# Kernel optimization log

Measured on AMD Instinct MI355X. Metric: run time of the kernel, lower is better.

## Reference

```python
import jax, jax.numpy as jnp
import numpy as np

BSZ, L, D = 8, 2048, 1024

def setup_inputs() -> dict:
    key = jax.random.key(0)
    k1, k2, k3, k4 = jax.random.split(key, 4)
    s = 1.0 / np.sqrt(D)
    return {
        "x":   jax.random.normal(k1, (BSZ, L, D), dtype=jnp.float32),
        "A":   jax.random.normal(k2, (D,), dtype=jnp.float32),
        "W_B": jax.random.normal(k3, (D, D), dtype=jnp.float32) * s,
        "b_B": jnp.zeros((D,), dtype=jnp.float32),
        "W_C": jax.random.normal(k4, (D, D), dtype=jnp.float32) * s,
        "b_C": jnp.zeros((D,), dtype=jnp.float32),
    }

def reference(x, A, W_B, b_B, W_C, b_C):
    # Precompute B(x_t) for all t in one GEMM: [B, L, D]
    Bx = jnp.einsum("bld,ed->ble", x, W_B) + b_B
    h0 = jnp.zeros((x.shape[0], x.shape[2]), dtype=x.dtype)

    def step(h, bx_t):
        h = jnp.tanh(A * h + bx_t)   # elementwise recurrence
        return h, h

    # scan over time: Bx -> [L, B, D]
    _, hs = jax.lax.scan(step, h0, jnp.swapaxes(Bx, 0, 1))
    # y_t = C(h_t), batched over all t: hs [L, B, D]
    y = jnp.einsum("lbd,ed->lbe", hs, W_C) + b_C
    return jnp.swapaxes(y, 0, 1)  # [B, L, D]
```

## Files before the change

kernel.cpp:

```cpp
#include <hip/hip_runtime.h>
#include <hip/hip_bf16.h>
#include <stdint.h>


using half8 = __attribute__((ext_vector_type(8))) _Float16;
using f32x4 = __attribute__((ext_vector_type(4))) float;

#define DEV __device__ __forceinline__

#if __has_builtin(__builtin_amdgcn_exp2f)
DEV float pexp(float x) { return __builtin_amdgcn_exp2f(x); }
constexpr float BX_SCALE = 2.8853900817779268f;
#else
DEV float pexp(float x) { return __expf(x); }
constexpr float BX_SCALE = 2.0f;
#endif

DEV ushort f2h(float x) {
  union { _Float16 f; ushort u; } c;
  c.f = (_Float16)x;
  return c.u;
}
DEV float h2f(ushort u) {
  union { ushort u; _Float16 f; } c;
  c.u = u;
  return (float)c.f;
}

DEV void gload_lds16(const void* g, void* l) {
  __builtin_amdgcn_global_load_lds((const __attribute__((address_space(1))) void*)g,
                                   (__attribute__((address_space(3))) void*)l,
                                   16, 0, 0);
}

__global__ void k_convert_all(const float* __restrict__ X, const float* __restrict__ WB,
                              const float* __restrict__ WC,
                              ushort* __restrict__ xh, ushort* __restrict__ xl,
                              ushort* __restrict__ wbh, ushort* __restrict__ wbl,
                              ushort* __restrict__ wch, int n4x, int n4w) {
  const int stride = gridDim.x * blockDim.x;
  const int total = n4x + 2 * n4w;
  for (int i = blockIdx.x * blockDim.x + threadIdx.x; i < total; i += stride) {
    if (i < n4x) {
      float4 v = reinterpret_cast<const float4*>(X)[i];
      ushort4 hv, lv;
      hv.x = f2h(v.x); lv.x = f2h(v.x - h2f(hv.x));
      hv.y = f2h(v.y); lv.y = f2h(v.y - h2f(hv.y));
      hv.z = f2h(v.z); lv.z = f2h(v.z - h2f(hv.z));
      hv.w = f2h(v.w); lv.w = f2h(v.w - h2f(hv.w));
      reinterpret_cast<ushort4*>(xh)[i] = hv;
      reinterpret_cast<ushort4*>(xl)[i] = lv;
    } else if (i < n4x + n4w) {
      const int j = i - n4x;
      float4 v = reinterpret_cast<const float4*>(WB)[j];
      ushort4 hv, lv;
      hv.x = f2h(v.x); lv.x = f2h(v.x - h2f(hv.x));
      hv.y = f2h(v.y); lv.y = f2h(v.y - h2f(hv.y));
      hv.z = f2h(v.z); lv.z = f2h(v.z - h2f(hv.z));
      hv.w = f2h(v.w); lv.w = f2h(v.w - h2f(hv.w));
      reinterpret_cast<ushort4*>(wbh)[j] = hv;
      reinterpret_cast<ushort4*>(wbl)[j] = lv;
    } else {
      const int j = i - n4x - n4w;
      float4 v = reinterpret_cast<const float4*>(WC)[j];
      ushort4 hv;
      hv.x = f2h(v.x); hv.y = f2h(v.y);
      hv.z = f2h(v.z); hv.w = f2h(v.w);
      reinterpret_cast<ushort4*>(wch)[j] = hv;
    }
  }
}

template <int SPLIT, int SCALE, int MINWAVES>
__global__ __launch_bounds__(256, MINWAVES)
void k_gemm_bt(const ushort* __restrict__ Ah, const ushort* __restrict__ Al,
               const ushort* __restrict__ Bh, const ushort* __restrict__ Bl,
               const float* __restrict__ bias, const float* __restrict__ Avec,
               float* __restrict__ C, int M, int N, int K) {
  constexpr int NMAT = SPLIT ? 4 : 2;
  __shared__ __align__(1024) ushort lds[NMAT * 128 * 64];
  ushort* sAh = lds;
  ushort* sAl = lds + (SPLIT ? 8192 : 0);
  ushort* sBh = lds + (SPLIT ? 16384 : 8192);
  ushort* sBl = lds + (SPLIT ? 24576 : 8192);

  const int t = threadIdx.x;
  const int lane = t & 63;
  const int w = t >> 6;
  const int wm = w >> 1, wn = w & 1;

  int bm, bn;
  {
    const int l = blockIdx.y * 8 + blockIdx.x;
    const int xcd = l & 7, s = l >> 3;
    bm = ((s >> 3) << 3) | xcd;
    bn = s & 7;
  }

  const int lr = lane & 15;
  const int lk = (lane >> 4) << 3;

  const ushort* gA_h = Ah + (size_t)(bm * 128) * K;
  const ushort* gA_l = SPLIT ? (Al + (size_t)(bm * 128) * K) : gA_h;
  const ushort* gB_h = Bh + (size_t)(bn * 128) * K;
  const ushort* gB_l = SPLIT ? (Bl + (size_t)(bn * 128) * K) : gB_h;

  f32x4 acc[4][4];
#pragma unroll
  for (int i = 0; i < 4; ++i)
#pragma unroll
    for (int j = 0; j < 4; ++j)
#pragma unroll
      for (int r = 0; r < 4; ++r) acc[i][j][r] = 0.f;

  auto stage = [&](int kt) {
    const int k0 = kt * 64;
#pragma unroll
    for (int i = 0; i < 4; ++i) {
      const int lin16 = i * 256 + t;
      const int lb = lin16 << 4;
      const int row = lb >> 7;
      const int srcb = (lb & 127) ^ ((row & 7) << 4);
      const size_t goff = (size_t)row * K + (size_t)(k0 + (srcb >> 1));
      const int lidx = i * 2048 + w * 512;
      gload_lds16(gA_h + goff, sAh + lidx);
      if (SPLIT) gload_lds16(gA_l + goff, sAl + lidx);
      gload_lds16(gB_h + goff, sBh + lidx);
      if (SPLIT) gload_lds16(gB_l + goff, sBl + lidx);
    }
  };

  auto ldfrag = [&](const ushort* s, int row, int kc) -> half8 {
    const int byte = (row << 7) + (((kc << 1) ^ ((row & 7) << 4)));
    return *reinterpret_cast<const half8*>(reinterpret_cast<const char*>(s) + byte);
  };

  const int NT = K / 64;
  stage(0);
  for (int kt = 0; kt < NT; ++kt) {
    __syncthreads();
#pragma unroll
    for (int kk = 0; kk < 2; ++kk) {
      half8 ah[4], bh[4], al[4], bl[4];
      const int kc = kk * 32 + lk;
#pragma unroll
      for (int i = 0; i < 4; ++i) {
        const int row = wm * 64 + i * 16 + lr;
        ah[i] = ldfrag(sAh, row, kc);
        if (SPLIT) al[i] = ldfrag(sAl, row, kc);
      }
#pragma unroll
      for (int j = 0; j < 4; ++j) {
        const int row = wn * 64 + j * 16 + lr;
        bh[j] = ldfrag(sBh, row, kc);
        if (SPLIT) bl[j] = ldfrag(sBl, row, kc);
      }
#pragma unroll
      for (int i = 0; i < 4; ++i)
#pragma unroll
        for (int j = 0; j < 4; ++j) {
          acc[i][j] = __builtin_amdgcn_mfma_f32_16x16x32_f16(ah[i], bh[j], acc[i][j], 0, 0, 0);
          if (SPLIT) {
            acc[i][j] = __builtin_amdgcn_mfma_f32_16x16x32_f16(al[i], bh[j], acc[i][j], 0, 0, 0);
            acc[i][j] = __builtin_amdgcn_mfma_f32_16x16x32_f16(ah[i], bl[j], acc[i][j], 0, 0, 0);
          }
        }
    }
    __syncthreads();
    if (kt + 1 < NT) stage(kt + 1);
  }

  float* Cb = C + (size_t)(bm * 128) * N + bn * 128;
#pragma unroll
  for (int i = 0; i < 4; ++i)
#pragma unroll
    for (int j = 0; j < 4; ++j) {
      const int col = wn * 64 + j * 16 + lr;
      float bv = bias[bn * 128 + col];
      if (SCALE) bv += Avec[bn * 128 + col];
#pragma unroll
      for (int r = 0; r < 4; ++r) {
        const int rowt = wm * 64 + i * 16 + ((lane >> 4) << 2) + r;
        float o = acc[i][j][r] + bv;
        if (SCALE) o *= BX_SCALE;
        Cb[(size_t)rowt * N + col] = o;
      }
    }
}

__global__ __launch_bounds__(64)
void k_recurrence(const float* __restrict__ Bx2, const float* __restrict__ Avec,
                  ushort* __restrict__ Hout) {
  const int tid = blockIdx.x * 64 + threadIdx.x;
  const int b = tid >> 10;
  const int d = tid & 1023;
  const float na2 = -2.f * BX_SCALE * Avec[d];
  const float* bx = Bx2 + (size_t)b * 2048 * 1024 + d;
  ushort* ho = Hout + (size_t)b * 2048 * 1024 + d;

  constexpr int P = 32;
  constexpr int NC = 2048 / P;
  float cA[P], cB[P];
#pragma unroll
  for (int i = 0; i < P; ++i) cA[i] = bx[(size_t)i * 1024];
#pragma unroll
  for (int i = 0; i < P; ++i) cB[i] = bx[(size_t)(P + i) * 1024];

  float r = 0.5f;
  for (int c = 0; c < NC; c += 2) {
#pragma unroll
    for (int i = 0; i < P; ++i) {
      const float u2 = fmaf(na2, r, cA[i]);
      r = __builtin_amdgcn_rcpf(pexp(u2) + 1.f);
      ho[(size_t)(c * P + i) * 1024] = f2h(fmaf(-2.f, r, 1.f));
    }
    if (c + 2 < NC) {
#pragma unroll
      for (int i = 0; i < P; ++i) cA[i] = bx[(size_t)((c + 2) * P + i) * 1024];
    }
#pragma unroll
    for (int i = 0; i < P; ++i) {
      const float u2 = fmaf(na2, r, cB[i]);
      r = __builtin_amdgcn_rcpf(pexp(u2) + 1.f);
      ho[(size_t)((c + 1) * P + i) * 1024] = f2h(fmaf(-2.f, r, 1.f));
    }
    if (c + 3 < NC) {
#pragma unroll
      for (int i = 0; i < P; ++i) cB[i] = bx[(size_t)((c + 3) * P + i) * 1024];
    }
  }
}

extern "C" void kernel_launch(void* const* d_in, const int* in_sizes, int n_in,
                              void* d_out, int out_size, void* d_ws, size_t ws_size,
                              hipStream_t stream) {
  const float* x   = (const float*)d_in[0];
  const float* A   = (const float*)d_in[1];
  const float* W_B = (const float*)d_in[2];
  const float* b_B = (const float*)d_in[3];
  const float* W_C = (const float*)d_in[4];
  const float* b_C = (const float*)d_in[5];
  float* y = (float*)d_out;

  const int Bsz = 8, L = 2048, D = 1024;
  const int M = Bsz * L;

  char* ws = (char*)d_ws;
  ushort* x_hi = (ushort*)(ws);
  ushort* x_lo = (ushort*)(ws + 33554432);
  ushort* wbh  = (ushort*)(ws + 67108864);
  ushort* wbl  = (ushort*)(ws + 69206016);
  ushort* wch  = (ushort*)(ws + 71303168);
  float*  Bx   = (float*)(ws + 73400320);
  ushort* h    = x_hi;

  k_convert_all<<<2048, 256, 0, stream>>>(x, W_B, W_C, x_hi, x_lo, wbh, wbl, wch,
                                          M * D / 4, D * D / 4);

  k_gemm_bt<1, 1, 2><<<dim3(8, M / 128), 256, 0, stream>>>(
      x_hi, x_lo, wbh, wbl, b_B, A, Bx, M, D, D);

  k_recurrence<<<(Bsz * D) / 64, 64, 0, stream>>>(Bx, A, h);

  k_gemm_bt<0, 0, 4><<<dim3(8, M / 128), 256, 0, stream>>>(
      h, (const ushort*)nullptr, wch, (const ushort*)nullptr, b_C,
      (const float*)nullptr, y, M, D, D);
}
```

Baseline: 230.1 us.

## Double-buffer LDS tiles with K=32 stages to overlap global loads with MFMA

Replaces the single-buffer K=64 staging loop with a two-buffer K=32 pipeline. The next tile is loaded straight into LDS while MFMAs run on the current one, and each iteration needs one barrier instead of two. The LDS layout is also reorganized: two rows are packed per 128-byte line with a new XOR swizzle, so the fragment reads match the narrower K tile. This should hide global load latency behind compute and cut barrier stalls. The cost is more loop iterations, each doing less MFMA work.

```diff
diff --git a/kernel.cpp b/kernel.cpp
--- a/kernel.cpp
+++ b/kernel.cpp
@@ -78,11 +78,7 @@
                const float* __restrict__ bias, const float* __restrict__ Avec,
                float* __restrict__ C, int M, int N, int K) {
   constexpr int NMAT = SPLIT ? 4 : 2;
-  __shared__ __align__(1024) ushort lds[NMAT * 128 * 64];
-  ushort* sAh = lds;
-  ushort* sAl = lds + (SPLIT ? 8192 : 0);
-  ushort* sBh = lds + (SPLIT ? 16384 : 8192);
-  ushort* sBl = lds + (SPLIT ? 24576 : 8192);
+  __shared__ __align__(1024) ushort lds[2 * NMAT * 4096];
 
   const int t = threadIdx.x;
   const int lane = t & 63;
@@ -98,7 +94,7 @@
   }
 
   const int lr = lane & 15;
-  const int lk = (lane >> 4) << 3;
+  const int kcb = (lane >> 4) << 4;
 
   const ushort* gA_h = Ah + (size_t)(bm * 128) * K;
   const ushort* gA_l = SPLIT ? (Al + (size_t)(bm * 128) * K) : gA_h;
@@ -113,61 +109,71 @@
 #pragma unroll
       for (int r = 0; r < 4; ++r) acc[i][j][r] = 0.f;
 
-  auto stage = [&](int kt) {
-    const int k0 = kt * 64;
+  auto stage = [&](int kt, int buf) {
+    const int k0 = kt * 32;
+    ushort* base = lds + buf * (NMAT * 4096);
+#pragma unroll
+    for (int i = 0; i < 2; ++i) {
+      const int lin16 = i * 256 + t;
+      const int line = lin16 >> 3;
+      const int row = (line << 1) | ((lin16 >> 2) & 1);
+      const int kb = ((lin16 & 3) << 4) ^ ((line & 3) << 4);
+      const size_t goff = (size_t)row * K + (size_t)(k0 + (kb >> 1));
+      const int dst = lin16 << 3;
+      gload_lds16(gA_h + goff, base + dst);
+      gload_lds16(gB_h + goff, base + (SPLIT ? 2 : 1) * 4096 + dst);
+      if (SPLIT) {
+        gload_lds16(gA_l + goff, base + 4096 + dst);
+        gload_lds16(gB_l + goff, base + 3 * 4096 + dst);
+      }
+    }
+  };
+
+  auto ldfrag = [&](const ushort* mat, int row) -> half8 {
+    const int line = row >> 1;
+    const int off = (line << 7) + ((row & 1) << 6) + (kcb ^ ((line & 3) << 4));
+    return *reinterpret_cast<const half8*>(reinterpret_cast<const char*>(mat) + off);
+  };
+
+  auto compute = [&](int buf) {
+    const ushort* base = lds + buf * (NMAT * 4096);
+    const ushort* sAh = base;
+    const ushort* sAl = base + 4096;
+    const ushort* sBh = base + (SPLIT ? 2 : 1) * 4096;
+    const ushort* sBl = base + 3 * 4096;
+
+    half8 ah[4], al[4], bh[4], bl[4];
 #pragma unroll
     for (int i = 0; i < 4; ++i) {
-      const int lin16 = i * 256 + t;
-      const int lb = lin16 << 4;
-      const int row = lb >> 7;
-      const int srcb = (lb & 127) ^ ((row & 7) << 4);
-      const size_t goff = (size_t)row * K + (size_t)(k0 + (srcb >> 1));
-      const int lidx = i * 2048 + w * 512;
-      gload_lds16(gA_h + goff, sAh + lidx);
-      if (SPLIT) gload_lds16(gA_l + goff, sAl + lidx);
-      gload_lds16(gB_h + goff, sBh + lidx);
-      if (SPLIT) gload_lds16(gB_l + goff, sBl + lidx);
-    }
+      const int r = wm * 64 + i * 16 + lr;
+      ah[i] = ldfrag(sAh, r);
+      if (SPLIT) al[i] = ldfrag(sAl, r);
+    }
+#pragma unroll
+    for (int j = 0; j < 4; ++j) {
+      const int r = wn * 64 + j * 16 + lr;
+      bh[j] = ldfrag(sBh, r);
+      if (SPLIT) bl[j] = ldfrag(sBl, r);
+    }
+#pragma unroll
+    for (int i = 0; i < 4; ++i)
+#pragma unroll
+      for (int j = 0; j < 4; ++j) {
+        acc[i][j] = __builtin_amdgcn_mfma_f32_16x16x32_f16(ah[i], bh[j], acc[i][j], 0, 0, 0);
+        if (SPLIT) {
+          acc[i][j] = __builtin_amdgcn_mfma_f32_16x16x32_f16(al[i], bh[j], acc[i][j], 0, 0, 0);
+          acc[i][j] = __builtin_amdgcn_mfma_f32_16x16x32_f16(ah[i], bl[j], acc[i][j], 0, 0, 0);
+        }
+      }
   };
 
-  auto ldfrag = [&](const ushort* s, int row, int kc) -> half8 {
-    const int byte = (row << 7) + (((kc << 1) ^ ((row & 7) << 4)));
-    return *reinterpret_cast<const half8*>(reinterpret_cast<const char*>(s) + byte);
-  };
-
-  const int NT = K / 64;
-  stage(0);
+  const int NT = K / 32;
+  stage(0, 0);
+  __syncthreads();
   for (int kt = 0; kt < NT; ++kt) {
+    if (kt + 1 < NT) stage(kt + 1, (kt + 1) & 1);
+    compute(kt & 1);
     __syncthreads();
-#pragma unroll
-    for (int kk = 0; kk < 2; ++kk) {
-      half8 ah[4], bh[4], al[4], bl[4];
-      const int kc = kk * 32 + lk;
-#pragma unroll
-      for (int i = 0; i < 4; ++i) {
-        const int row = wm * 64 + i * 16 + lr;
-        ah[i] = ldfrag(sAh, row, kc);
-        if (SPLIT) al[i] = ldfrag(sAl, row, kc);
-      }
-#pragma unroll
-      for (int j = 0; j < 4; ++j) {
-        const int row = wn * 64 + j * 16 + lr;
-        bh[j] = ldfrag(sBh, row, kc);
-        if (SPLIT) bl[j] = ldfrag(sBl, row, kc);
-      }
-#pragma unroll
-      for (int i = 0; i < 4; ++i)
-#pragma unroll
-        for (int j = 0; j < 4; ++j) {
-          acc[i][j] = __builtin_amdgcn_mfma_f32_16x16x32_f16(ah[i], bh[j], acc[i][j], 0, 0, 0);
-          if (SPLIT) {
-            acc[i][j] = __builtin_amdgcn_mfma_f32_16x16x32_f16(al[i], bh[j], acc[i][j], 0, 0, 0);
-            acc[i][j] = __builtin_amdgcn_mfma_f32_16x16x32_f16(ah[i], bl[j], acc[i][j], 0, 0, 0);
-          }
-        }
-    }
-    __syncthreads();
-    if (kt + 1 < NT) stage(kt + 1);
   }
 
   float* Cb = C + (size_t)(bm * 128) * N + bn * 128;
```

After: 248.5 us. 8.0% more time.

## Double-buffer LDS tiles in GEMM kernels with vmcnt-based prefetch pipelining

Applied to the files above, without the earlier changes.

Gives both GEMM kernels two LDS buffers and prefetches the tile two steps ahead. A partial s_waitcnt on vmcnt lets the next tile's global-to-LDS loads overlap MFMA compute on the current one, where the old loop had a full sync between load and use. This doubles LDS use per block (128KB for the split GEMM, 64KB for the plain one), so the launch-bounds occupancy hints are halved. The tradeoff is fewer resident waves in exchange for overlapping loads with compute.

```diff
diff --git a/kernel.cpp b/kernel.cpp
--- a/kernel.cpp
+++ b/kernel.cpp
@@ -78,11 +78,7 @@
                const float* __restrict__ bias, const float* __restrict__ Avec,
                float* __restrict__ C, int M, int N, int K) {
   constexpr int NMAT = SPLIT ? 4 : 2;
-  __shared__ __align__(1024) ushort lds[NMAT * 128 * 64];
-  ushort* sAh = lds;
-  ushort* sAl = lds + (SPLIT ? 8192 : 0);
-  ushort* sBh = lds + (SPLIT ? 16384 : 8192);
-  ushort* sBl = lds + (SPLIT ? 24576 : 8192);
+  __shared__ __align__(1024) ushort lds[2 * NMAT * 8192];
 
   const int t = threadIdx.x;
   const int lane = t & 63;
@@ -113,8 +109,9 @@
 #pragma unroll
       for (int r = 0; r < 4; ++r) acc[i][j][r] = 0.f;
 
-  auto stage = [&](int kt) {
+  auto stage = [&](int kt, int buf) {
     const int k0 = kt * 64;
+    ushort* base = lds + buf * (NMAT * 8192);
 #pragma unroll
     for (int i = 0; i < 4; ++i) {
       const int lin16 = i * 256 + t;
@@ -123,10 +120,10 @@
       const int srcb = (lb & 127) ^ ((row & 7) << 4);
       const size_t goff = (size_t)row * K + (size_t)(k0 + (srcb >> 1));
       const int lidx = i * 2048 + w * 512;
-      gload_lds16(gA_h + goff, sAh + lidx);
-      if (SPLIT) gload_lds16(gA_l + goff, sAl + lidx);
-      gload_lds16(gB_h + goff, sBh + lidx);
-      if (SPLIT) gload_lds16(gB_l + goff, sBl + lidx);
+      gload_lds16(gA_h + goff, base + lidx);
+      if (SPLIT) gload_lds16(gA_l + goff, base + 8192 + lidx);
+      gload_lds16(gB_h + goff, base + (SPLIT ? 2 : 1) * 8192 + lidx);
+      if (SPLIT) gload_lds16(gB_l + goff, base + 3 * 8192 + lidx);
     }
   };
 
@@ -135,10 +132,12 @@
     return *reinterpret_cast<const half8*>(reinterpret_cast<const char*>(s) + byte);
   };
 
-  const int NT = K / 64;
-  stage(0);
-  for (int kt = 0; kt < NT; ++kt) {
-    __syncthreads();
+  auto compute = [&](int buf) {
+    const ushort* base = lds + buf * (NMAT * 8192);
+    const ushort* sAh = base;
+    const ushort* sAl = base + 8192;
+    const ushort* sBh = base + (SPLIT ? 2 : 1) * 8192;
+    const ushort* sBl = base + 3 * 8192;
 #pragma unroll
     for (int kk = 0; kk < 2; ++kk) {
       half8 ah[4], bh[4], al[4], bl[4];
@@ -166,8 +165,24 @@
           }
         }
     }
-    __syncthreads();
-    if (kt + 1 < NT) stage(kt + 1);
+  };
+
+  const int NT = K / 64;
+  stage(0, 0);
+  stage(1, 1);
+  for (int kt = 0; kt < NT; ++kt) {
+    if (kt + 1 < NT) {
+      if (SPLIT) asm volatile("s_waitcnt vmcnt(16)" ::: "memory");
+      else       asm volatile("s_waitcnt vmcnt(8)" ::: "memory");
+    } else {
+      asm volatile("s_waitcnt vmcnt(0)" ::: "memory");
+    }
+    __builtin_amdgcn_s_barrier();
+    __builtin_amdgcn_sched_barrier(0);
+    compute(kt & 1);
+    __builtin_amdgcn_s_barrier();
+    __builtin_amdgcn_sched_barrier(0);
+    if (kt + 2 < NT) stage(kt + 2, kt & 1);
   }
 
   float* Cb = C + (size_t)(bm * 128) * N + bn * 128;
@@ -257,12 +272,12 @@
   k_convert_all<<<2048, 256, 0, stream>>>(x, W_B, W_C, x_hi, x_lo, wbh, wbl, wch,
                                           M * D / 4, D * D / 4);
 
-  k_gemm_bt<1, 1, 2><<<dim3(8, M / 128), 256, 0, stream>>>(
+  k_gemm_bt<1, 1, 1><<<dim3(8, M / 128), 256, 0, stream>>>(
       x_hi, x_lo, wbh, wbl, b_B, A, Bx, M, D, D);
 
   k_recurrence<<<(Bsz * D) / 64, 64, 0, stream>>>(Bx, A, h);
 
-  k_gemm_bt<0, 0, 4><<<dim3(8, M / 128), 256, 0, stream>>>(
+  k_gemm_bt<0, 0, 2><<<dim3(8, M / 128), 256, 0, stream>>>(
       h, (const ushort*)nullptr, wch, (const ushort*)nullptr, b_C,
       (const float*)nullptr, y, M, D, D);
 }
```

New measurement: 257.6 us. 11.9% more time.

## Pipeline time chunks so recurrence overlaps with both GEMMs in fused launches

Applied to the files above, without the earlier changes.

The sequence dimension is split into four 512-step chunks. One combined kernel runs three roles per launch: the recurrence on chunk c, the input GEMM on chunk c+1 and the output GEMM on chunk c-1. The recurrence carries its hidden state between launches through a workspace buffer. This hides the latency-bound serial scan behind the GEMM work. In exchange there are more launches, the recurrence blocks now share CUs with GEMM blocks, and launch bounds and register limits are shared across all roles.

```diff
diff --git a/kernel.cpp b/kernel.cpp
--- a/kernel.cpp
+++ b/kernel.cpp
@@ -71,14 +71,12 @@
   }
 }
 
-template <int SPLIT, int SCALE, int MINWAVES>
-__global__ __launch_bounds__(256, MINWAVES)
-void k_gemm_bt(const ushort* __restrict__ Ah, const ushort* __restrict__ Al,
-               const ushort* __restrict__ Bh, const ushort* __restrict__ Bl,
-               const float* __restrict__ bias, const float* __restrict__ Avec,
-               float* __restrict__ C, int M, int N, int K) {
-  constexpr int NMAT = SPLIT ? 4 : 2;
-  __shared__ __align__(1024) ushort lds[NMAT * 128 * 64];
+template <int SPLIT, int SCALE>
+DEV void gemm_role(const ushort* __restrict__ Ah, const ushort* __restrict__ Al,
+                   const ushort* __restrict__ Bh, const ushort* __restrict__ Bl,
+                   const float* __restrict__ bias, const float* __restrict__ Avec,
+                   float* __restrict__ C, int chunk, int g, ushort* lds) {
+  constexpr int K = 1024, N = 1024;
   ushort* sAh = lds;
   ushort* sAl = lds + (SPLIT ? 8192 : 0);
   ushort* sBh = lds + (SPLIT ? 16384 : 8192);
@@ -89,13 +87,10 @@
   const int w = t >> 6;
   const int wm = w >> 1, wn = w & 1;
 
-  int bm, bn;
-  {
-    const int l = blockIdx.y * 8 + blockIdx.x;
-    const int xcd = l & 7, s = l >> 3;
-    bm = ((s >> 3) << 3) | xcd;
-    bn = s & 7;
-  }
+  const int xcd = g & 7, s = g >> 3;
+  const int tc = (s & ~7) | xcd;
+  const int bn = s & 7;
+  const int bm = ((tc >> 2) << 4) + chunk * 4 + (tc & 3);
 
   const int lr = lane & 15;
   const int lk = (lane >> 4) << 3;
@@ -130,9 +125,9 @@
     }
   };
 
-  auto ldfrag = [&](const ushort* s, int row, int kc) -> half8 {
+  auto ldfrag = [&](const ushort* sp, int row, int kc) -> half8 {
     const int byte = (row << 7) + (((kc << 1) ^ ((row & 7) << 4)));
-    return *reinterpret_cast<const half8*>(reinterpret_cast<const char*>(s) + byte);
+    return *reinterpret_cast<const half8*>(reinterpret_cast<const char*>(sp) + byte);
   };
 
   const int NT = K / 64;
@@ -188,25 +183,25 @@
     }
 }
 
-__global__ __launch_bounds__(64)
-void k_recurrence(const float* __restrict__ Bx2, const float* __restrict__ Avec,
-                  ushort* __restrict__ Hout) {
-  const int tid = blockIdx.x * 64 + threadIdx.x;
+DEV void rec_role(const float* __restrict__ Bx2, const float* __restrict__ Avec,
+                  ushort* __restrict__ Hout, float* __restrict__ hs,
+                  int cr, int rbid) {
+  const int tid = rbid * 256 + (int)threadIdx.x;
   const int b = tid >> 10;
   const int d = tid & 1023;
   const float na2 = -2.f * BX_SCALE * Avec[d];
-  const float* bx = Bx2 + (size_t)b * 2048 * 1024 + d;
-  ushort* ho = Hout + (size_t)b * 2048 * 1024 + d;
+  const float* bx = Bx2 + (size_t)(b * 2048 + cr * 512) * 1024 + d;
+  ushort* ho = Hout + (size_t)(b * 2048 + cr * 512) * 1024 + d;
 
   constexpr int P = 32;
-  constexpr int NC = 2048 / P;
+  constexpr int NC = 512 / P;
   float cA[P], cB[P];
 #pragma unroll
   for (int i = 0; i < P; ++i) cA[i] = bx[(size_t)i * 1024];
 #pragma unroll
   for (int i = 0; i < P; ++i) cB[i] = bx[(size_t)(P + i) * 1024];
 
-  float r = 0.5f;
+  float r = (cr == 0) ? 0.5f : hs[tid];
   for (int c = 0; c < NC; c += 2) {
 #pragma unroll
     for (int i = 0; i < P; ++i) {
@@ -229,6 +224,31 @@
       for (int i = 0; i < P; ++i) cB[i] = bx[(size_t)((c + 3) * P + i) * 1024];
     }
   }
+  hs[tid] = r;
+}
+
+__global__ __launch_bounds__(256, 2)
+void k_combo(const ushort* __restrict__ xh, const ushort* __restrict__ xl,
+             const ushort* __restrict__ wbh, const ushort* __restrict__ wbl,
+             const ushort* __restrict__ wch,
+             const float* __restrict__ bB, const float* __restrict__ bC,
+             const float* __restrict__ Avec,
+             float* __restrict__ Bx, ushort* __restrict__ h,
+             float* __restrict__ hs, float* __restrict__ y,
+             int cr, int c1, int nr, int c2) {
+  extern __shared__ ushort lds[];
+  int bid = blockIdx.x;
+  if (bid < nr) { rec_role(Bx, Avec, h, hs, cr, bid); return; }
+  bid -= nr;
+  if (c1 >= 0) {
+    if (bid < 256) {
+      gemm_role<1, 1>(xh, xl, wbh, wbl, bB, Avec, Bx, c1, bid, lds);
+      return;
+    }
+    bid -= 256;
+  }
+  gemm_role<0, 0>(h, (const ushort*)nullptr, wch, (const ushort*)nullptr,
+                  bC, (const float*)nullptr, y, c2, bid, lds);
 }
 
 extern "C" void kernel_launch(void* const* d_in, const int* in_sizes, int n_in,
@@ -252,17 +272,25 @@
   ushort* wbl  = (ushort*)(ws + 69206016);
   ushort* wch  = (ushort*)(ws + 71303168);
   float*  Bx   = (float*)(ws + 73400320);
+  float*  hs   = (float*)(ws + 140509184);
   ushort* h    = x_hi;
 
   k_convert_all<<<2048, 256, 0, stream>>>(x, W_B, W_C, x_hi, x_lo, wbh, wbl, wch,
                                           M * D / 4, D * D / 4);
 
-  k_gemm_bt<1, 1, 2><<<dim3(8, M / 128), 256, 0, stream>>>(
-      x_hi, x_lo, wbh, wbl, b_B, A, Bx, M, D, D);
-
-  k_recurrence<<<(Bsz * D) / 64, 64, 0, stream>>>(Bx, A, h);
-
-  k_gemm_bt<0, 0, 4><<<dim3(8, M / 128), 256, 0, stream>>>(
-      h, (const ushort*)nullptr, wch, (const ushort*)nullptr, b_C,
-      (const float*)nullptr, y, M, D, D);
-}
+  auto combo = [&](int cr, int c1, int c2) {
+    const int nr = (cr >= 0) ? 32 : 0;
+    const int n1 = (c1 >= 0) ? 256 : 0;
+    const int n2 = (c2 >= 0) ? 256 : 0;
+    const size_t sh = (c1 >= 0) ? 65536 : 32768;
+    k_combo<<<nr + n1 + n2, 256, sh, stream>>>(
+        x_hi, x_lo, wbh, wbl, wch, b_B, b_C, A, Bx, h, hs, y, cr, c1, nr, c2);
+  };
+
+  combo(-1, 0, -1);
+  combo( 0, 1, -1);
+  combo( 1, 2,  0);
+  combo( 2, 3,  1);
+  combo( 3, -1, 2);
+  combo(-1, -1, 3);
+}
```

Result: no change. 233.8 us (+1.6%).
